# Performance work log

Measured on AMD Instinct MI355X. Metric: run time of the kernel, lower is better.

The kernel has to match this reference:

```python
import jax, jax.numpy as jnp
import numpy as np

B, PROB, POMO = 16, 2048, 256      # batch, problem size (nodes), pomo (queries)
E, H, D = 128, 8, 16               # embedding_dim, head_num, qkv_dim (H*D == E)
NE, K = 8, 2                       # num_experts, top-k
SQRT_E = float(np.sqrt(E))
CLIP = 10.0
EPS = 1e-10


def setup_inputs() -> dict:
    key = jax.random.key(0)
    ks = jax.random.split(key, 12)
    s = 0.08  # weight init scale ~ 1/sqrt(fan_in)
    return {
        "encoded_nodes": jax.random.normal(ks[0], (B, PROB, E), jnp.float32),
        "encoded_last_node": jax.random.normal(ks[1], (B, POMO, E), jnp.float32),
        "mid_embd_pref": jax.random.normal(ks[2], (B, E), jnp.float32),
        "load": jax.random.uniform(ks[3], (B, POMO), jnp.float32),
        "ninf_mask": jnp.zeros((B, POMO, PROB), jnp.float32),
        "Wq_last": jax.random.normal(ks[4], (E + 1, H * D), jnp.float32) * s,
        "Wk": jax.random.normal(ks[5], (E, H * D), jnp.float32) * s,
        "Wv": jax.random.normal(ks[6], (E, H * D), jnp.float32) * s,
        "expert_W": jax.random.normal(ks[7], (NE, H * D, E), jnp.float32) * s,
        "expert_b": jax.random.normal(ks[8], (NE, E), jnp.float32) * 0.01,
        "w_gate": jax.random.normal(ks[9], (E, NE), jnp.float32) * s,
    }


def _heads(x):  # [B, n, H*D] -> [B, H, n, D]
    b, n, _ = x.shape
    return x.reshape(b, n, H, D).transpose(0, 2, 1, 3)


def _cv_squared(x):
    m = jnp.mean(x)
    v = jnp.var(x)
    return v / (m * m + EPS)


def reference(encoded_nodes, encoded_last_node, mid_embd_pref, load, ninf_mask,
              Wq_last, Wk, Wv, expert_W, expert_b, w_gate):
    # ---- set_kv ----
    k = _heads(encoded_nodes @ Wk)   # [B,H,PROB,D]
    v = _heads(encoded_nodes @ Wv)   # [B,H,PROB,D]

    # ---- single-step multi-head attention ----
    input_cat = jnp.concatenate([encoded_last_node, load[:, :, None]], axis=2)  # [B,POMO,E+1]
    q = _heads(input_cat @ Wq_last)  # [B,H,POMO,D]
    score = jnp.einsum("bhpd,bhnd->bhpn", q, k) / jnp.sqrt(jnp.float32(D))
    score = score + ninf_mask[:, None, :, :]
    weights = jax.nn.softmax(score, axis=3)
    out = jnp.einsum("bhpn,bhnd->bhpd", weights, v)
    out_concat = out.transpose(0, 2, 1, 3).reshape(B, POMO, H * D)  # [B,POMO,E]

    # ---- MoE combine (problem-level noisy top-k gating, eval/clean logits) ----
    gate_logits = mid_embd_pref @ w_gate               # [B,NE]
    top_logits, top_idx = jax.lax.top_k(gate_logits, K)
    top_gates = jax.nn.softmax(top_logits, axis=-1)    # T = 1.0
    gates = jnp.zeros((B, NE), out_concat.dtype).at[jnp.arange(B)[:, None], top_idx].set(top_gates)
    expert_out = jnp.einsum("bpd,edh->bpeh", out_concat, expert_W) + expert_b[None, None]
    mh_atten_out = jnp.einsum("bpeh,be->bph", expert_out, gates)   # [B,POMO,E]
    importance = gates.sum(0)
    exp_load = (gates > 0).astype(jnp.float32).sum(0)
    moe_loss = _cv_squared(importance) + _cv_squared(exp_load)

    # ---- clipped-logit masked softmax over problem nodes ----
    score2 = jnp.einsum("bph,bnh->bpn", mh_atten_out, encoded_nodes) / SQRT_E
    score_clipped = CLIP * jnp.tanh(score2)
    probs = jax.nn.softmax(score_clipped + ninf_mask, axis=2)  # [B,POMO,PROB]
    return probs, moe_loss
```

## Files before the change

kernel.cpp:

```cpp
#include <hip/hip_runtime.h>
#include <math.h>

#define BB    16
#define PROBN 2048
#define POMO  256
#define ED    128
#define HN    8
#define DDIM  16
#define NEXP  8

typedef _Float16 f16;
typedef f16 f16x2 __attribute__((ext_vector_type(2)));

__device__ __forceinline__ f16x2 f2h(float f) {
  union U { float f; f16x2 h; } u; u.f = f; return u.h;
}
__device__ __forceinline__ float packh2(float a, float b) {
  union U { float f; f16x2 h; } u; u.h.x = (f16)a; u.h.y = (f16)b; return u.f;
}
__device__ __forceinline__ float fdot2f(f16x2 a, f16x2 b, float c) {
#if __has_builtin(__builtin_amdgcn_fdot2)
  return __builtin_amdgcn_fdot2(a, b, c, false);
#else
  return c + (float)a.x * (float)b.x + (float)a.y * (float)b.y;
#endif
}

#define WS_KH    0
#define WS_VHT   (WS_KH + 2097152)
#define WS_NH    (WS_VHT + 2097152)
#define WS_QH    (WS_NH + 2097152)
#define WS_OUT   (WS_QH + 262144)
#define WS_MH    (WS_OUT + 524288)
#define WS_WC    (WS_MH + 524288)
#define WS_BC    (WS_WC + 262144)
#define WS_GATES (WS_BC + 2048)

__global__ __launch_bounds__(128) void k_gating(
    const float* __restrict__ mid, const float* __restrict__ w_gate,
    float* __restrict__ gates_ws, float* __restrict__ moe_out)
{
  __shared__ float lg[BB][NEXP];
  __shared__ float gt[BB][NEXP];
  int t = threadIdx.x;
  {
    int b = t >> 3, e = t & 7;
    float acc = 0.f;
    #pragma unroll 8
    for (int k = 0; k < ED; ++k) acc += mid[b*ED + k] * w_gate[k*NEXP + e];
    lg[b][e] = acc;
  }
  __syncthreads();
  if (t < BB) {
    int b = t;
    int i1 = 0; float v1 = lg[b][0];
    #pragma unroll
    for (int e = 1; e < NEXP; ++e) if (lg[b][e] > v1) { v1 = lg[b][e]; i1 = e; }
    int i2 = -1; float v2 = -3.0e38f;
    #pragma unroll
    for (int e = 0; e < NEXP; ++e) if (e != i1 && lg[b][e] > v2) { v2 = lg[b][e]; i2 = e; }
    float e2 = __expf(v2 - v1);
    float g1 = 1.f / (1.f + e2);
    #pragma unroll
    for (int e = 0; e < NEXP; ++e) gt[b][e] = 0.f;
    gt[b][i1] = g1;
    gt[b][i2] = e2 * g1;
  }
  __syncthreads();
  if (t < BB*NEXP) gates_ws[t] = gt[t >> 3][t & 7];
  if (t == 0) {
    float imp[NEXP], ldc[NEXP];
    #pragma unroll
    for (int e = 0; e < NEXP; ++e) { imp[e] = 0.f; ldc[e] = 0.f; }
    for (int b = 0; b < BB; ++b)
      #pragma unroll
      for (int e = 0; e < NEXP; ++e) {
        float g = gt[b][e];
        imp[e] += g;
        if (g > 0.f) ldc[e] += 1.f;
      }
    float im = 0.f, lm = 0.f;
    #pragma unroll
    for (int e = 0; e < NEXP; ++e) { im += imp[e]; lm += ldc[e]; }
    im *= 0.125f; lm *= 0.125f;
    float iv = 0.f, lv = 0.f;
    #pragma unroll
    for (int e = 0; e < NEXP; ++e) {
      float a = imp[e] - im; iv += a*a;
      float c = ldc[e] - lm; lv += c*c;
    }
    iv *= 0.125f; lv *= 0.125f;
    moe_out[0] = iv / (im*im + 1e-10f) + lv / (lm*lm + 1e-10f);
  }
}

__global__ __launch_bounds__(256) void k_experts(
    const float* __restrict__ gates, const float* __restrict__ eW,
    const float* __restrict__ eB, float* __restrict__ WC, float* __restrict__ BC)
{
  __shared__ float g[NEXP];
  int tid = threadIdx.x;
  int b = blockIdx.x >> 3;
  int tile = blockIdx.x & 7;
  if (tid < NEXP) g[tid] = gates[b*NEXP + tid];
  __syncthreads();
  int i0 = tile * 2048;
  #pragma unroll
  for (int j = 0; j < 8; ++j) {
    int i = i0 + tid + j*256;
    float a = 0.f;
    #pragma unroll
    for (int e = 0; e < NEXP; ++e) a += g[e] * eW[e*ED*ED + i];
    WC[b*ED*ED + i] = a;
  }
  if (tile == 0 && tid < ED) {
    float a = 0.f;
    #pragma unroll
    for (int e = 0; e < NEXP; ++e) a += g[e] * eB[e*ED + tid];
    BC[b*ED + tid] = a;
  }
}

__global__ __launch_bounds__(256) void k_kv(
    const float* __restrict__ nodes, const float* __restrict__ Wk,
    const float* __restrict__ Wv, float* __restrict__ Khf,
    float* __restrict__ VhTf, float* __restrict__ Nhf)
{
  __shared__ __align__(16) float As[64*132];
  __shared__ __align__(16) float Wks[32*128];
  __shared__ __align__(16) float Wvs[32*128];
  int tid = threadIdx.x;
  int r0 = blockIdx.x * 64;
  #pragma unroll
  for (int j = 0; j < 8; ++j) {
    int idx = tid + j*256;
    int row = idx >> 5, c4 = (idx & 31) << 2;
    float4 v = *(const float4*)&nodes[(size_t)(r0 + row)*ED + c4];
    *(float4*)&As[row*132 + c4] = v;
    float2 nh; nh.x = packh2(v.x, v.y); nh.y = packh2(v.z, v.w);
    *(float2*)&Nhf[(size_t)(r0 + row)*64 + (c4 >> 1)] = nh;
  }
  int colg = tid & 15, rowg = tid >> 4;
  int c0 = colg << 2;
  float accK[4][8], accV[4][8];
  #pragma unroll
  for (int i = 0; i < 4; ++i)
    #pragma unroll
    for (int j = 0; j < 8; ++j) { accK[i][j] = 0.f; accV[i][j] = 0.f; }

  for (int kk = 0; kk < 128; kk += 32) {
    __syncthreads();
    #pragma unroll
    for (int j = 0; j < 4; ++j) {
      int idx = tid + j*256;
      int row = idx >> 5, c4 = (idx & 31) << 2;
      *(float4*)&Wks[row*128 + c4] = *(const float4*)&Wk[(kk + row)*ED + c4];
      *(float4*)&Wvs[row*128 + c4] = *(const float4*)&Wv[(kk + row)*ED + c4];
    }
    __syncthreads();
    #pragma unroll 4
    for (int k = 0; k < 32; ++k) {
      float a[4];
      #pragma unroll
      for (int i = 0; i < 4; ++i) a[i] = As[(rowg*4 + i)*132 + kk + k];
      float4 wk0 = *(float4*)&Wks[k*128 + c0];
      float4 wk1 = *(float4*)&Wks[k*128 + c0 + 64];
      float4 wv0 = *(float4*)&Wvs[k*128 + c0];
      float4 wv1 = *(float4*)&Wvs[k*128 + c0 + 64];
      #pragma unroll
      for (int i = 0; i < 4; ++i) {
        accK[i][0] += a[i]*wk0.x; accK[i][1] += a[i]*wk0.y;
        accK[i][2] += a[i]*wk0.z; accK[i][3] += a[i]*wk0.w;
        accK[i][4] += a[i]*wk1.x; accK[i][5] += a[i]*wk1.y;
        accK[i][6] += a[i]*wk1.z; accK[i][7] += a[i]*wk1.w;
        accV[i][0] += a[i]*wv0.x; accV[i][1] += a[i]*wv0.y;
        accV[i][2] += a[i]*wv0.z; accV[i][3] += a[i]*wv0.w;
        accV[i][4] += a[i]*wv1.x; accV[i][5] += a[i]*wv1.y;
        accV[i][6] += a[i]*wv1.z; accV[i][7] += a[i]*wv1.w;
      }
    }
  }
  #pragma unroll
  for (int i = 0; i < 4; ++i) {
    size_t row = (size_t)(r0 + rowg*4 + i);
    float2 k0; k0.x = packh2(accK[i][0], accK[i][1]); k0.y = packh2(accK[i][2], accK[i][3]);
    float2 k1; k1.x = packh2(accK[i][4], accK[i][5]); k1.y = packh2(accK[i][6], accK[i][7]);
    *(float2*)&Khf[row*64 + (c0 >> 1)]      = k0;
    *(float2*)&Khf[row*64 + (c0 >> 1) + 32] = k1;
  }
  int bb = r0 >> 11;
  int nn0 = (r0 & 2047) + rowg*4;
  #pragma unroll
  for (int j = 0; j < 8; ++j) {
    int col = (j < 4) ? (c0 + j) : (c0 + 60 + j);
    float2 vv; vv.x = packh2(accV[0][j], accV[1][j]); vv.y = packh2(accV[2][j], accV[3][j]);
    *(float2*)&VhTf[((size_t)bb*128 + col)*1024 + (nn0 >> 1)] = vv;
  }
}

__global__ __launch_bounds__(256) void k_q(
    const float* __restrict__ last, const float* __restrict__ loadv,
    const float* __restrict__ Wq, float* __restrict__ Qhf)
{
  __shared__ __align__(16) float As[32*132];
  __shared__ __align__(16) float Ws[129*128];
  int tid = threadIdx.x;
  int r0 = blockIdx.x * 32;
  #pragma unroll
  for (int j = 0; j < 4; ++j) {
    int idx = tid + j*256;
    int row = idx >> 5, c4 = (idx & 31) << 2;
    *(float4*)&As[row*132 + c4] = *(const float4*)&last[(size_t)(r0 + row)*ED + c4];
  }
  if (tid < 32) As[tid*132 + 128] = loadv[r0 + tid];
  for (int idx = tid; idx < 4128; idx += 256)
    *(float4*)&Ws[idx*4] = *(const float4*)&Wq[idx*4];
  __syncthreads();

  int colg = tid & 15, rowg = tid >> 4;
  int c0 = colg << 2;
  float acc[2][8];
  #pragma unroll
  for (int i = 0; i < 2; ++i)
    #pragma unroll
    for (int j = 0; j < 8; ++j) acc[i][j] = 0.f;
  #pragma unroll 4
  for (int k = 0; k < 129; ++k) {
    float a0 = As[(rowg*2)*132 + k];
    float a1 = As[(rowg*2 + 1)*132 + k];
    float4 w0 = *(float4*)&Ws[k*128 + c0];
    float4 w1 = *(float4*)&Ws[k*128 + c0 + 64];
    acc[0][0] += a0*w0.x; acc[0][1] += a0*w0.y; acc[0][2] += a0*w0.z; acc[0][3] += a0*w0.w;
    acc[0][4] += a0*w1.x; acc[0][5] += a0*w1.y; acc[0][6] += a0*w1.z; acc[0][7] += a0*w1.w;
    acc[1][0] += a1*w0.x; acc[1][1] += a1*w0.y; acc[1][2] += a1*w0.z; acc[1][3] += a1*w0.w;
    acc[1][4] += a1*w1.x; acc[1][5] += a1*w1.y; acc[1][6] += a1*w1.z; acc[1][7] += a1*w1.w;
  }
  #pragma unroll
  for (int i = 0; i < 2; ++i) {
    size_t row = (size_t)(r0 + rowg*2 + i);
    float2 q0; q0.x = packh2(acc[i][0], acc[i][1]); q0.y = packh2(acc[i][2], acc[i][3]);
    float2 q1; q1.x = packh2(acc[i][4], acc[i][5]); q1.y = packh2(acc[i][6], acc[i][7]);
    *(float2*)&Qhf[row*64 + (c0 >> 1)]      = q0;
    *(float2*)&Qhf[row*64 + (c0 >> 1) + 32] = q1;
  }
}

__global__ __launch_bounds__(256, 4) void k_attn(
    const float* __restrict__ Khf, const float* __restrict__ VhTf,
    const float* __restrict__ Qhf, const float* __restrict__ mask,
    float* __restrict__ Op)
{
  __shared__ __align__(16) float kt[64*20];
  __shared__ __align__(16) float vt[16*68];
  int tid = threadIdx.x;
  int h = blockIdx.x & 7, b = blockIdx.x >> 3;
  int ph = blockIdx.y;
  int nq = tid & 15;
  int pg = tid >> 4;
  int prow0 = b*POMO + ph*32 + pg*2;
  const float* maskb = mask + (size_t)prow0 * PROBN;
  const float* Kb = Khf + (size_t)b*PROBN*64 + h*8;
  const float* Vb = VhTf + ((size_t)b*128 + h*16)*1024;

  f16x2 q[2][8];
  #pragma unroll
  for (int qi = 0; qi < 2; ++qi) {
    const float* qp = Qhf + (size_t)(prow0 + qi)*64 + h*8;
    float4 t0 = *(const float4*)&qp[0];
    float4 t1 = *(const float4*)&qp[4];
    q[qi][0] = f2h(t0.x); q[qi][1] = f2h(t0.y); q[qi][2] = f2h(t0.z); q[qi][3] = f2h(t0.w);
    q[qi][4] = f2h(t1.x); q[qi][5] = f2h(t1.y); q[qi][6] = f2h(t1.z); q[qi][7] = f2h(t1.w);
  }
  float m[2], l[2], acc[2][16];
  #pragma unroll
  for (int qi = 0; qi < 2; ++qi) {
    m[qi] = -1.0e30f; l[qi] = 0.f;
    #pragma unroll
    for (int dd = 0; dd < 16; ++dd) acc[qi][dd] = 0.f;
  }

  int srow = tid >> 1, part = tid & 1;
  int kws = 20*(srow >> 1) + 8*(srow & 1) + 4*part;
  int vrow = tid >> 4, vchunk = tid & 15;
  int vws = 68*vrow + 4*vchunk;

  for (int tile = 0; tile < 16; ++tile) {
    int t0 = tile << 7;
    if (tile > 0) __syncthreads();
    *(float4*)&kt[kws] = *(const float4*)&Kb[(size_t)(t0 + srow)*64 + part*4];
    *(float4*)&vt[vws] = *(const float4*)&Vb[(size_t)vrow*1024 + (t0 >> 1) + vchunk*4];
    __syncthreads();

    float s[2][8];
    #pragma unroll
    for (int qi = 0; qi < 2; ++qi)
      #pragma unroll
      for (int i = 0; i < 4; ++i) {
        s[qi][2*i]   = maskb[(size_t)qi*PROBN + t0 + 2*nq + 32*i];
        s[qi][2*i+1] = maskb[(size_t)qi*PROBN + t0 + 2*nq + 32*i + 1];
      }
    #pragma unroll
    for (int i = 0; i < 4; ++i) {
      int p = nq + 16*i;
      float4 a0 = *(float4*)&kt[20*p];
      float4 a1 = *(float4*)&kt[20*p + 4];
      float4 b0 = *(float4*)&kt[20*p + 8];
      float4 b1 = *(float4*)&kt[20*p + 12];
      f16x2 ka[8] = {f2h(a0.x), f2h(a0.y), f2h(a0.z), f2h(a0.w),
                     f2h(a1.x), f2h(a1.y), f2h(a1.z), f2h(a1.w)};
      f16x2 kb[8] = {f2h(b0.x), f2h(b0.y), f2h(b0.z), f2h(b0.w),
                     f2h(b1.x), f2h(b1.y), f2h(b1.z), f2h(b1.w)};
      #pragma unroll
      for (int qi = 0; qi < 2; ++qi) {
        float d0 = 0.f, d1 = 0.f;
        #pragma unroll
        for (int j = 0; j < 8; ++j) {
          d0 = fdot2f(q[qi][j], ka[j], d0);
          d1 = fdot2f(q[qi][j], kb[j], d1);
        }
        s[qi][2*i]   += d0 * 0.25f;
        s[qi][2*i+1] += d1 * 0.25f;
      }
    }
    #pragma unroll
    for (int qi = 0; qi < 2; ++qi) {
      float tm = s[qi][0];
      #pragma unroll
      for (int i = 1; i < 8; ++i) tm = fmaxf(tm, s[qi][i]);
      float M = fmaxf(m[qi], tm);
      float c = __expf(m[qi] - M);
      m[qi] = M;
      l[qi] *= c;
      #pragma unroll
      for (int dd = 0; dd < 16; ++dd) acc[qi][dd] *= c;
    }
    #pragma unroll
    for (int i = 0; i < 4; ++i) {
      int p = nq + 16*i;
      f16x2 wp0, wp1;
      {
        float w0 = __expf(s[0][2*i] - m[0]);
        float w1 = __expf(s[0][2*i+1] - m[0]);
        l[0] += w0 + w1;
        wp0.x = (f16)w0; wp0.y = (f16)w1;
        float u0 = __expf(s[1][2*i] - m[1]);
        float u1 = __expf(s[1][2*i+1] - m[1]);
        l[1] += u0 + u1;
        wp1.x = (f16)u0; wp1.y = (f16)u1;
      }
      #pragma unroll
      for (int dd = 0; dd < 16; ++dd) {
        f16x2 vh = f2h(vt[68*dd + p]);
        acc[0][dd] = fdot2f(wp0, vh, acc[0][dd]);
        acc[1][dd] = fdot2f(wp1, vh, acc[1][dd]);
      }
    }
  }

  #pragma unroll
  for (int off = 1; off < 16; off <<= 1) {
    #pragma unroll
    for (int qi = 0; qi < 2; ++qi) {
      float m2 = __shfl_xor(m[qi], off);
      float l2 = __shfl_xor(l[qi], off);
      float M = fmaxf(m[qi], m2);
      float c1 = __expf(m[qi] - M), c2 = __expf(m2 - M);
      l[qi] = l[qi]*c1 + l2*c2;
      m[qi] = M;
      #pragma unroll
      for (int dd = 0; dd < 16; ++dd) {
        float a2 = __shfl_xor(acc[qi][dd], off);
        acc[qi][dd] = acc[qi][dd]*c1 + a2*c2;
      }
    }
  }
  #pragma unroll
  for (int d4 = 0; d4 < 4; ++d4) {
    if (nq == d4) {
      #pragma unroll
      for (int qi = 0; qi < 2; ++qi) {
        float rl = 1.f / l[qi];
        *(float4*)&Op[(size_t)(prow0 + qi)*ED + h*16 + d4*4] =
          make_float4(acc[qi][4*d4+0]*rl, acc[qi][4*d4+1]*rl,
                      acc[qi][4*d4+2]*rl, acc[qi][4*d4+3]*rl);
      }
    }
  }
}

__global__ __launch_bounds__(256) void k_mh(
    const float* __restrict__ Op, const float* __restrict__ WC,
    const float* __restrict__ BC, float* __restrict__ MH)
{
  __shared__ __align__(16) float As[32*132];
  __shared__ __align__(16) float Ws[128*128];
  int tid = threadIdx.x;
  int b = blockIdx.x >> 3;
  int pt = blockIdx.x & 7;
  int r0 = b*POMO + pt*32;
  #pragma unroll
  for (int j = 0; j < 4; ++j) {
    int idx = tid + j*256;
    int row = idx >> 5, c4 = (idx & 31) << 2;
    *(float4*)&As[row*132 + c4] = *(const float4*)&Op[(size_t)(r0 + row)*ED + c4];
  }
  for (int idx = tid; idx < 4096; idx += 256)
    *(float4*)&Ws[idx*4] = *(const float4*)&WC[(size_t)b*ED*ED + idx*4];
  __syncthreads();

  int colg = tid & 15, rowg = tid >> 4;
  int c0 = colg << 2;
  float4 b0 = *(const float4*)&BC[b*ED + c0];
  float4 b1 = *(const float4*)&BC[b*ED + c0 + 64];
  float acc[2][8];
  #pragma unroll
  for (int i = 0; i < 2; ++i) {
    acc[i][0] = b0.x; acc[i][1] = b0.y; acc[i][2] = b0.z; acc[i][3] = b0.w;
    acc[i][4] = b1.x; acc[i][5] = b1.y; acc[i][6] = b1.z; acc[i][7] = b1.w;
  }
  #pragma unroll 4
  for (int k = 0; k < 128; ++k) {
    float a0 = As[(rowg*2)*132 + k];
    float a1 = As[(rowg*2 + 1)*132 + k];
    float4 w0 = *(float4*)&Ws[k*128 + c0];
    float4 w1 = *(float4*)&Ws[k*128 + c0 + 64];
    acc[0][0] += a0*w0.x; acc[0][1] += a0*w0.y; acc[0][2] += a0*w0.z; acc[0][3] += a0*w0.w;
    acc[0][4] += a0*w1.x; acc[0][5] += a0*w1.y; acc[0][6] += a0*w1.z; acc[0][7] += a0*w1.w;
    acc[1][0] += a1*w0.x; acc[1][1] += a1*w0.y; acc[1][2] += a1*w0.z; acc[1][3] += a1*w0.w;
    acc[1][4] += a1*w1.x; acc[1][5] += a1*w1.y; acc[1][6] += a1*w1.z; acc[1][7] += a1*w1.w;
  }
  #pragma unroll
  for (int i = 0; i < 2; ++i) {
    size_t row = (size_t)(r0 + rowg*2 + i) * ED;
    *(float4*)&MH[row + c0]      = make_float4(acc[i][0], acc[i][1], acc[i][2], acc[i][3]);
    *(float4*)&MH[row + c0 + 64] = make_float4(acc[i][4], acc[i][5], acc[i][6], acc[i][7]);
  }
}

__global__ __launch_bounds__(256) void k_final(
    const float* __restrict__ MH, const float* __restrict__ Nhf,
    const float* __restrict__ mask, float* __restrict__ probs)
{
  __shared__ __align__(16) float lg[8*PROBN];
  __shared__ __align__(16) float mh8[8*68];
  int tid = threadIdx.x;
  int b = blockIdx.x >> 5;
  int p0 = (blockIdx.x & 31) * 8;
  {
    int row = tid >> 5, c4 = (tid & 31) << 2;
    float4 v = *(const float4*)&MH[(size_t)(b*POMO + p0 + row)*ED + c4];
    float2 hh; hh.x = packh2(v.x, v.y); hh.y = packh2(v.z, v.w);
    *(float2*)&mh8[row*68 + (c4 >> 1)] = hh;
  }
  __syncthreads();
  const float invs = 0.08838834764831845f;
  #pragma unroll
  for (int j = 0; j < 8; ++j) {
    int n = tid + (j << 8);
    const float* nr = &Nhf[(size_t)(b*PROBN + n)*64];
    float a[8];
    #pragma unroll
    for (int p = 0; p < 8; ++p) a[p] = 0.f;
    #pragma unroll 4
    for (int kq = 0; kq < 16; ++kq) {
      float4 nv = *(const float4*)&nr[kq*4];
      f16x2 n0 = f2h(nv.x), n1 = f2h(nv.y), n2 = f2h(nv.z), n3 = f2h(nv.w);
      #pragma unroll
      for (int p = 0; p < 8; ++p) {
        float4 mv = *(const float4*)&mh8[p*68 + kq*4];
        a[p] = fdot2f(f2h(mv.x), n0, a[p]);
        a[p] = fdot2f(f2h(mv.y), n1, a[p]);
        a[p] = fdot2f(f2h(mv.z), n2, a[p]);
        a[p] = fdot2f(f2h(mv.w), n3, a[p]);
      }
    }
    #pragma unroll
    for (int p = 0; p < 8; ++p) lg[p*PROBN + n] = a[p] * invs;
  }
  __syncthreads();

  int wid = tid >> 6, lane = tid & 63;
  #pragma unroll
  for (int pp = 0; pp < 2; ++pp) {
    int p = wid*2 + pp;
    const float* mrow = mask + (size_t)(b*POMO + p0 + p) * PROBN;
    float* prow = probs + (size_t)(b*POMO + p0 + p) * PROBN;
    float z[32];
    float mx = -3.0e38f;
    #pragma unroll
    for (int i4 = 0; i4 < 8; ++i4) {
      int n = 4*lane + 256*i4;
      float4 lv = *(const float4*)&lg[p*PROBN + n];
      float4 mv = *(const float4*)&mrow[n];
      float z0 = 10.f - 20.f/(__expf(2.f*lv.x)+1.f) + mv.x;
      float z1 = 10.f - 20.f/(__expf(2.f*lv.y)+1.f) + mv.y;
      float z2 = 10.f - 20.f/(__expf(2.f*lv.z)+1.f) + mv.z;
      float z3 = 10.f - 20.f/(__expf(2.f*lv.w)+1.f) + mv.w;
      z[4*i4+0] = z0; z[4*i4+1] = z1; z[4*i4+2] = z2; z[4*i4+3] = z3;
      mx = fmaxf(fmaxf(fmaxf(mx, z0), fmaxf(z1, z2)), z3);
    }
    #pragma unroll
    for (int off = 32; off > 0; off >>= 1) mx = fmaxf(mx, __shfl_xor(mx, off));
    float sum = 0.f;
    #pragma unroll
    for (int k = 0; k < 32; ++k) { z[k] = __expf(z[k] - mx); sum += z[k]; }
    #pragma unroll
    for (int off = 32; off > 0; off >>= 1) sum += __shfl_xor(sum, off);
    float rs = 1.f / sum;
    #pragma unroll
    for (int i4 = 0; i4 < 8; ++i4) {
      int n = 4*lane + 256*i4;
      *(float4*)&prow[n] = make_float4(z[4*i4+0]*rs, z[4*i4+1]*rs,
                                       z[4*i4+2]*rs, z[4*i4+3]*rs);
    }
  }
}

extern "C" void kernel_launch(void* const* d_in, const int* in_sizes, int n_in,
                              void* d_out, int out_size, void* d_ws, size_t ws_size,
                              hipStream_t stream)
{
  const float* nodes  = (const float*)d_in[0];
  const float* last   = (const float*)d_in[1];
  const float* mid    = (const float*)d_in[2];
  const float* loadv  = (const float*)d_in[3];
  const float* mask   = (const float*)d_in[4];
  const float* Wq     = (const float*)d_in[5];
  const float* Wk     = (const float*)d_in[6];
  const float* Wv     = (const float*)d_in[7];
  const float* eW     = (const float*)d_in[8];
  const float* eB     = (const float*)d_in[9];
  const float* w_gate = (const float*)d_in[10];
  float* out = (float*)d_out;
  float* ws  = (float*)d_ws;

  k_gating<<<1, 128, 0, stream>>>(mid, w_gate, ws + WS_GATES, out + BB*POMO*PROBN);
  k_experts<<<128, 256, 0, stream>>>(ws + WS_GATES, eW, eB, ws + WS_WC, ws + WS_BC);
  k_kv<<<512, 256, 0, stream>>>(nodes, Wk, Wv, ws + WS_KH, ws + WS_VHT, ws + WS_NH);
  k_q<<<128, 256, 0, stream>>>(last, loadv, Wq, ws + WS_QH);
  k_attn<<<dim3(128, 8), 256, 0, stream>>>(ws + WS_KH, ws + WS_VHT, ws + WS_QH, mask, ws + WS_OUT);
  k_mh<<<128, 256, 0, stream>>>(ws + WS_OUT, ws + WS_WC, ws + WS_BC, ws + WS_MH);
  k_final<<<512, 256, 0, stream>>>(ws + WS_MH, ws + WS_NH, mask, out);
}
```

Before: 192.7 us.

## Convert K/V projection, attention output and expert GEMM to packed fp16 dot2

The K/V projection, the expert-combined weight matrix and the attention output are now stored as packed half pairs, and the two small GEMMs use fdot2 with fp32 accumulation in place of scalar FMAs. k_mh moves to 16-row tiles across twice as many blocks, and its shared memory footprint shrinks. The aim is to halve LDS and global traffic and the FMA instruction count in these stages. In exchange, inputs and weights lose precision to fp16 before the dot products.

```diff
diff --git a/kernel.cpp b/kernel.cpp
--- a/kernel.cpp
+++ b/kernel.cpp
@@ -31,9 +31,9 @@
 #define WS_NH    (WS_VHT + 2097152)
 #define WS_QH    (WS_NH + 2097152)
 #define WS_OUT   (WS_QH + 262144)
-#define WS_MH    (WS_OUT + 524288)
+#define WS_MH    (WS_OUT + 262144)
 #define WS_WC    (WS_MH + 524288)
-#define WS_BC    (WS_WC + 262144)
+#define WS_BC    (WS_WC + 131072)
 #define WS_GATES (WS_BC + 2048)
 
 __global__ __launch_bounds__(128) void k_gating(
@@ -96,7 +96,7 @@
 
 __global__ __launch_bounds__(256) void k_experts(
     const float* __restrict__ gates, const float* __restrict__ eW,
-    const float* __restrict__ eB, float* __restrict__ WC, float* __restrict__ BC)
+    const float* __restrict__ eB, float* __restrict__ WCh, float* __restrict__ BC)
 {
   __shared__ float g[NEXP];
   int tid = threadIdx.x;
@@ -104,14 +104,19 @@
   int tile = blockIdx.x & 7;
   if (tid < NEXP) g[tid] = gates[b*NEXP + tid];
   __syncthreads();
-  int i0 = tile * 2048;
-  #pragma unroll
-  for (int j = 0; j < 8; ++j) {
-    int i = i0 + tid + j*256;
-    float a = 0.f;
-    #pragma unroll
-    for (int e = 0; e < NEXP; ++e) a += g[e] * eW[e*ED*ED + i];
-    WC[b*ED*ED + i] = a;
+  int i0 = tile * 1024;
+  #pragma unroll
+  for (int j = 0; j < 4; ++j) {
+    int pi = i0 + tid + j*256;
+    int k2 = (pi >> 7) << 1;
+    int c  = pi & 127;
+    float a0 = 0.f, a1 = 0.f;
+    #pragma unroll
+    for (int e = 0; e < NEXP; ++e) {
+      a0 += g[e] * eW[e*ED*ED + k2*ED + c];
+      a1 += g[e] * eW[e*ED*ED + (k2+1)*ED + c];
+    }
+    WCh[(size_t)b*8192 + pi] = packh2(a0, a1);
   }
   if (tile == 0 && tid < ED) {
     float a = 0.f;
@@ -126,9 +131,9 @@
     const float* __restrict__ Wv, float* __restrict__ Khf,
     float* __restrict__ VhTf, float* __restrict__ Nhf)
 {
-  __shared__ __align__(16) float As[64*132];
-  __shared__ __align__(16) float Wks[32*128];
-  __shared__ __align__(16) float Wvs[32*128];
+  __shared__ __align__(16) float Ash[64*66];
+  __shared__ __align__(16) float Wkp[16*128];
+  __shared__ __align__(16) float Wvp[16*128];
   int tid = threadIdx.x;
   int r0 = blockIdx.x * 64;
   #pragma unroll
@@ -136,8 +141,8 @@
     int idx = tid + j*256;
     int row = idx >> 5, c4 = (idx & 31) << 2;
     float4 v = *(const float4*)&nodes[(size_t)(r0 + row)*ED + c4];
-    *(float4*)&As[row*132 + c4] = v;
     float2 nh; nh.x = packh2(v.x, v.y); nh.y = packh2(v.z, v.w);
+    *(float2*)&Ash[row*66 + (c4 >> 1)] = nh;
     *(float2*)&Nhf[(size_t)(r0 + row)*64 + (c4 >> 1)] = nh;
   }
   int colg = tid & 15, rowg = tid >> 4;
@@ -151,32 +156,49 @@
   for (int kk = 0; kk < 128; kk += 32) {
     __syncthreads();
     #pragma unroll
-    for (int j = 0; j < 4; ++j) {
-      int idx = tid + j*256;
-      int row = idx >> 5, c4 = (idx & 31) << 2;
-      *(float4*)&Wks[row*128 + c4] = *(const float4*)&Wk[(kk + row)*ED + c4];
-      *(float4*)&Wvs[row*128 + c4] = *(const float4*)&Wv[(kk + row)*ED + c4];
+    for (int j = 0; j < 2; ++j) {
+      int wi = tid + j*256;
+      int p = wi >> 5, c4 = (wi & 31) << 2;
+      float4 ka = *(const float4*)&Wk[(kk + 2*p)*ED + c4];
+      float4 kb = *(const float4*)&Wk[(kk + 2*p + 1)*ED + c4];
+      float4 pk; pk.x = packh2(ka.x, kb.x); pk.y = packh2(ka.y, kb.y);
+      pk.z = packh2(ka.z, kb.z); pk.w = packh2(ka.w, kb.w);
+      *(float4*)&Wkp[p*128 + c4] = pk;
+      float4 va = *(const float4*)&Wv[(kk + 2*p)*ED + c4];
+      float4 vb = *(const float4*)&Wv[(kk + 2*p + 1)*ED + c4];
+      float4 pv; pv.x = packh2(va.x, vb.x); pv.y = packh2(va.y, vb.y);
+      pv.z = packh2(va.z, vb.z); pv.w = packh2(va.w, vb.w);
+      *(float4*)&Wvp[p*128 + c4] = pv;
     }
     __syncthreads();
     #pragma unroll 4
-    for (int k = 0; k < 32; ++k) {
-      float a[4];
-      #pragma unroll
-      for (int i = 0; i < 4; ++i) a[i] = As[(rowg*4 + i)*132 + kk + k];
-      float4 wk0 = *(float4*)&Wks[k*128 + c0];
-      float4 wk1 = *(float4*)&Wks[k*128 + c0 + 64];
-      float4 wv0 = *(float4*)&Wvs[k*128 + c0];
-      float4 wv1 = *(float4*)&Wvs[k*128 + c0 + 64];
+    for (int p = 0; p < 16; ++p) {
+      float ap[4];
+      #pragma unroll
+      for (int i = 0; i < 4; ++i) ap[i] = Ash[(rowg*4 + i)*66 + (kk >> 1) + p];
+      float4 wk0 = *(float4*)&Wkp[p*128 + c0];
+      float4 wk1 = *(float4*)&Wkp[p*128 + c0 + 64];
+      float4 wv0 = *(float4*)&Wvp[p*128 + c0];
+      float4 wv1 = *(float4*)&Wvp[p*128 + c0 + 64];
       #pragma unroll
       for (int i = 0; i < 4; ++i) {
-        accK[i][0] += a[i]*wk0.x; accK[i][1] += a[i]*wk0.y;
-        accK[i][2] += a[i]*wk0.z; accK[i][3] += a[i]*wk0.w;
-        accK[i][4] += a[i]*wk1.x; accK[i][5] += a[i]*wk1.y;
-        accK[i][6] += a[i]*wk1.z; accK[i][7] += a[i]*wk1.w;
-        accV[i][0] += a[i]*wv0.x; accV[i][1] += a[i]*wv0.y;
-        accV[i][2] += a[i]*wv0.z; accV[i][3] += a[i]*wv0.w;
-        accV[i][4] += a[i]*wv1.x; accV[i][5] += a[i]*wv1.y;
-        accV[i][6] += a[i]*wv1.z; accV[i][7] += a[i]*wv1.w;
+        f16x2 ai = f2h(ap[i]);
+        accK[i][0] = fdot2f(ai, f2h(wk0.x), accK[i][0]);
+        accK[i][1] = fdot2f(ai, f2h(wk0.y), accK[i][1]);
+        accK[i][2] = fdot2f(ai, f2h(wk0.z), accK[i][2]);
+        accK[i][3] = fdot2f(ai, f2h(wk0.w), accK[i][3]);
+        accK[i][4] = fdot2f(ai, f2h(wk1.x), accK[i][4]);
+        accK[i][5] = fdot2f(ai, f2h(wk1.y), accK[i][5]);
+        accK[i][6] = fdot2f(ai, f2h(wk1.z), accK[i][6]);
+        accK[i][7] = fdot2f(ai, f2h(wk1.w), accK[i][7]);
+        accV[i][0] = fdot2f(ai, f2h(wv0.x), accV[i][0]);
+        accV[i][1] = fdot2f(ai, f2h(wv0.y), accV[i][1]);
+        accV[i][2] = fdot2f(ai, f2h(wv0.z), accV[i][2]);
+        accV[i][3] = fdot2f(ai, f2h(wv0.w), accV[i][3]);
+        accV[i][4] = fdot2f(ai, f2h(wv1.x), accV[i][4]);
+        accV[i][5] = fdot2f(ai, f2h(wv1.y), accV[i][5]);
+        accV[i][6] = fdot2f(ai, f2h(wv1.z), accV[i][6]);
+        accV[i][7] = fdot2f(ai, f2h(wv1.w), accV[i][7]);
       }
     }
   }
@@ -248,7 +270,7 @@
 __global__ __launch_bounds__(256, 4) void k_attn(
     const float* __restrict__ Khf, const float* __restrict__ VhTf,
     const float* __restrict__ Qhf, const float* __restrict__ mask,
-    float* __restrict__ Op)
+    float* __restrict__ Oph)
 {
   __shared__ __align__(16) float kt[64*20];
   __shared__ __align__(16) float vt[16*68];
@@ -380,61 +402,58 @@
       #pragma unroll
       for (int qi = 0; qi < 2; ++qi) {
         float rl = 1.f / l[qi];
-        *(float4*)&Op[(size_t)(prow0 + qi)*ED + h*16 + d4*4] =
-          make_float4(acc[qi][4*d4+0]*rl, acc[qi][4*d4+1]*rl,
-                      acc[qi][4*d4+2]*rl, acc[qi][4*d4+3]*rl);
+        float2 o;
+        o.x = packh2(acc[qi][4*d4+0]*rl, acc[qi][4*d4+1]*rl);
+        o.y = packh2(acc[qi][4*d4+2]*rl, acc[qi][4*d4+3]*rl);
+        *(float2*)&Oph[(size_t)(prow0 + qi)*64 + h*8 + d4*2] = o;
       }
     }
   }
 }
 
 __global__ __launch_bounds__(256) void k_mh(
-    const float* __restrict__ Op, const float* __restrict__ WC,
+    const float* __restrict__ Oph, const float* __restrict__ WCh,
     const float* __restrict__ BC, float* __restrict__ MH)
 {
-  __shared__ __align__(16) float As[32*132];
-  __shared__ __align__(16) float Ws[128*128];
+  __shared__ __align__(16) float Ash[16*66];
+  __shared__ __align__(16) float Wp[64*128];
   int tid = threadIdx.x;
-  int b = blockIdx.x >> 3;
-  int pt = blockIdx.x & 7;
-  int r0 = b*POMO + pt*32;
-  #pragma unroll
-  for (int j = 0; j < 4; ++j) {
-    int idx = tid + j*256;
-    int row = idx >> 5, c4 = (idx & 31) << 2;
-    *(float4*)&As[row*132 + c4] = *(const float4*)&Op[(size_t)(r0 + row)*ED + c4];
-  }
-  for (int idx = tid; idx < 4096; idx += 256)
-    *(float4*)&Ws[idx*4] = *(const float4*)&WC[(size_t)b*ED*ED + idx*4];
+  int b = blockIdx.x >> 4;
+  int pt = blockIdx.x & 15;
+  int r0 = b*POMO + pt*16;
+  {
+    int row = tid >> 4, c4 = (tid & 15) << 2;
+    *(float4*)&Ash[row*66 + c4] = *(const float4*)&Oph[(size_t)(r0 + row)*64 + c4];
+  }
+  #pragma unroll
+  for (int j = 0; j < 8; ++j) {
+    int wi = tid + j*256;
+    *(float4*)&Wp[wi*4] = *(const float4*)&WCh[(size_t)b*8192 + wi*4];
+  }
   __syncthreads();
 
   int colg = tid & 15, rowg = tid >> 4;
   int c0 = colg << 2;
   float4 b0 = *(const float4*)&BC[b*ED + c0];
   float4 b1 = *(const float4*)&BC[b*ED + c0 + 64];
-  float acc[2][8];
-  #pragma unroll
-  for (int i = 0; i < 2; ++i) {
-    acc[i][0] = b0.x; acc[i][1] = b0.y; acc[i][2] = b0.z; acc[i][3] = b0.w;
-    acc[i][4] = b1.x; acc[i][5] = b1.y; acc[i][6] = b1.z; acc[i][7] = b1.w;
-  }
+  float acc[8] = {b0.x, b0.y, b0.z, b0.w, b1.x, b1.y, b1.z, b1.w};
   #pragma unroll 4
-  for (int k = 0; k < 128; ++k) {
-    float a0 = As[(rowg*2)*132 + k];
-    float a1 = As[(rowg*2 + 1)*132 + k];
-    float4 w0 = *(float4*)&Ws[k*128 + c0];
-    float4 w1 = *(float4*)&Ws[k*128 + c0 + 64];
-    acc[0][0] += a0*w0.x; acc[0][1] += a0*w0.y; acc[0][2] += a0*w0.z; acc[0][3] += a0*w0.w;
-    acc[0][4] += a0*w1.x; acc[0][5] += a0*w1.y; acc[0][6] += a0*w1.z; acc[0][7] += a0*w1.w;
-    acc[1][0] += a1*w0.x; acc[1][1] += a1*w0.y; acc[1][2] += a1*w0.z; acc[1][3] += a1*w0.w;
-    acc[1][4] += a1*w1.x; acc[1][5] += a1*w1.y; acc[1][6] += a1*w1.z; acc[1][7] += a1*w1.w;
-  }
-  #pragma unroll
-  for (int i = 0; i < 2; ++i) {
-    size_t row = (size_t)(r0 + rowg*2 + i) * ED;
-    *(float4*)&MH[row + c0]      = make_float4(acc[i][0], acc[i][1], acc[i][2], acc[i][3]);
-    *(float4*)&MH[row + c0 + 64] = make_float4(acc[i][4], acc[i][5], acc[i][6], acc[i][7]);
-  }
+  for (int p = 0; p < 64; ++p) {
+    f16x2 a = f2h(Ash[rowg*66 + p]);
+    float4 w0 = *(float4*)&Wp[p*128 + c0];
+    float4 w1 = *(float4*)&Wp[p*128 + c0 + 64];
+    acc[0] = fdot2f(a, f2h(w0.x), acc[0]);
+    acc[1] = fdot2f(a, f2h(w0.y), acc[1]);
+    acc[2] = fdot2f(a, f2h(w0.z), acc[2]);
+    acc[3] = fdot2f(a, f2h(w0.w), acc[3]);
+    acc[4] = fdot2f(a, f2h(w1.x), acc[4]);
+    acc[5] = fdot2f(a, f2h(w1.y), acc[5]);
+    acc[6] = fdot2f(a, f2h(w1.z), acc[6]);
+    acc[7] = fdot2f(a, f2h(w1.w), acc[7]);
+  }
+  size_t row = (size_t)(r0 + rowg) * ED;
+  *(float4*)&MH[row + c0]      = make_float4(acc[0], acc[1], acc[2], acc[3]);
+  *(float4*)&MH[row + c0 + 64] = make_float4(acc[4], acc[5], acc[6], acc[7]);
 }
 
 __global__ __launch_bounds__(256) void k_final(
@@ -539,6 +558,6 @@
   k_kv<<<512, 256, 0, stream>>>(nodes, Wk, Wv, ws + WS_KH, ws + WS_VHT, ws + WS_NH);
   k_q<<<128, 256, 0, stream>>>(last, loadv, Wq, ws + WS_QH);
   k_attn<<<dim3(128, 8), 256, 0, stream>>>(ws + WS_KH, ws + WS_VHT, ws + WS_QH, mask, ws + WS_OUT);
-  k_mh<<<128, 256, 0, stream>>>(ws + WS_OUT, ws + WS_WC, ws + WS_BC, ws + WS_MH);
+  k_mh<<<256, 256, 0, stream>>>(ws + WS_OUT, ws + WS_WC, ws + WS_BC, ws + WS_MH);
   k_final<<<512, 256, 0, stream>>>(ws + WS_MH, ws + WS_NH, mask, out);
 }
```

After: 182.2 us. -5.4%, faster.
